# Optimization experiments

Hardware: AMD Instinct MI355X
Metric: run time of the kernel (lower is better)

Reference implementation:

```python
import jax, jax.numpy as jnp
import numpy as np

NUM_EMBEDDINGS = 1024
EMBEDDING_DIM = 64
SCALE = 1.0 / NUM_EMBEDDINGS


def setup_inputs() -> dict:
    key = jax.random.key(0)
    k1, k2 = jax.random.split(key)
    input = jax.random.normal(k1, (16, EMBEDDING_DIM, 64, 64), dtype=jnp.float32)
    # nn.Embedding weight initialized uniform(-scale, scale)
    codebook = jax.random.uniform(k2, (NUM_EMBEDDINGS, EMBEDDING_DIM),
                                  dtype=jnp.float32, minval=-SCALE, maxval=SCALE)
    return {"input": input, "codebook": codebook}


def reference(input, codebook):
    # NCHW -> NHWC, flatten spatial+batch to tokens [N, D]
    x = jnp.transpose(input, (0, 2, 3, 1))           # [B, H, W, D]
    B, H, W, D = x.shape
    flat = x.reshape(-1, D)                          # [N, D]
    dists = (jnp.sum(flat ** 2, axis=1, keepdims=True)
             + jnp.sum(codebook ** 2, axis=1)
             - 2.0 * flat @ codebook.T)              # [N, K]
    idx = jnp.argmin(dists, axis=-1).reshape(B, H, W)  # [B, H, W]
    quantized = codebook[idx]                        # [B, H, W, D]
    return jnp.transpose(quantized, (0, 3, 1, 2))    # [B, D, H, W]
```

## Files before the change

### kernel.cpp

```cpp
#include <hip/hip_runtime.h>

typedef short short8 __attribute__((ext_vector_type(8)));
typedef float f32x4 __attribute__((ext_vector_type(4)));
typedef unsigned long long u64;

#define NE 1024
#define D 64
#define HW 4096
#define NTOK 65536
#define MARGIN 3.0e-3f
#define FLT_MAX_F 3.402823466e+38f

#define WS_BN  0
#define WS_EBF 4096
#define WS_WIN 135168

__device__ __forceinline__ unsigned short f2bf(float f) {
    unsigned u = __float_as_uint(f);
    return (unsigned short)((u + 0x7fffu + ((u >> 16) & 1u)) >> 16);
}

__device__ __forceinline__ unsigned fenc(float f) {
    unsigned u = __float_as_uint(f);
    return (u & 0x80000000u) ? ~u : (u | 0x80000000u);
}
__device__ __forceinline__ float fdec(unsigned u) {
    unsigned v = (u & 0x80000000u) ? (u & 0x7FFFFFFFu) : ~u;
    return __uint_as_float(v);
}

__device__ __forceinline__ float np_sum64_sq(const float* v) {
    float s[8];
#pragma unroll
    for (int j = 0; j < 8; ++j) s[j] = __fmul_rn(v[j], v[j]);
#pragma unroll
    for (int i = 8; i < 64; i += 8) {
#pragma unroll
        for (int j = 0; j < 8; ++j)
            s[j] = __fadd_rn(s[j], __fmul_rn(v[i + j], v[i + j]));
    }
    return __fadd_rn(__fadd_rn(__fadd_rn(s[0], s[1]), __fadd_rn(s[2], s[3])),
                     __fadd_rn(__fadd_rn(s[4], s[5]), __fadd_rn(s[6], s[7])));
}

__global__ __launch_bounds__(256) void kP_prep(
        const float* __restrict__ cb, float* __restrict__ bn,
        unsigned short* __restrict__ ebf, u64* __restrict__ mask,
        unsigned* __restrict__ gmin) {
    const int gid = blockIdx.x * 256 + threadIdx.x;
    int4 z = {0, 0, 0, 0};
    int4* mz = (int4*)mask;
#pragma unroll
    for (int i = 0; i < 8; ++i) mz[(size_t)gid * 8 + i] = z;
    gmin[gid] = 0xFFFFFFFFu;
    ebf[gid] = f2bf(cb[gid]);
    if (gid < NE) {
        float row[D];
        const float4* r4 = reinterpret_cast<const float4*>(cb + (size_t)gid * D);
#pragma unroll
        for (int i = 0; i < 16; ++i) {
            float4 v = r4[i];
            row[4*i+0] = v.x; row[4*i+1] = v.y; row[4*i+2] = v.z; row[4*i+3] = v.w;
        }
        bn[gid] = np_sum64_sq(row);
    }
}

#define K1_HEAD                                                               \
    __shared__ unsigned short ebq[128 * 64];                                  \
    __shared__ float sbn[128];                                                \
    const int sw  = (blockIdx.x & 7) * 512 + (blockIdx.x >> 3);               \
    const int tg  = sw >> 3;                                                  \
    const int c   = sw & 7;                                                   \
    const int tid  = threadIdx.x;                                             \
    const int lane = tid & 63, w = tid >> 6;                                  \
    const int lcol = lane & 15, lhi = lane >> 4, lrow = lhi * 4;              \
    const int tokw = tg * 128 + w * 32;                                       \
    if (tid < 128) sbn[tid] = bn_g[c * 128 + tid];                            \
    const char* src = (const char*)(ebf + (size_t)c * 128 * 64);              \
    _Pragma("unroll")                                                         \
    for (int i = 0; i < 4; ++i) {                                             \
        int L = (tid + i * 256) * 16;                                         \
        int row = L >> 7, wi = L & 127;                                       \
        int4 v = *(const int4*)(src + L);                                     \
        *(int4*)((char*)ebq + row * 128 + (wi ^ ((row & 7) << 4))) = v;       \
    }                                                                         \
    const int b = tokw >> 12, hwb = tokw & 4095;                              \
    const float* xbase = in + (size_t)b * (D * HW);                           \
    const int hw0 = hwb + lcol, hw1 = hw0 + 16;                               \
    const int kb = lhi * 8;                                                   \
    short8 B00, B01, B10, B11;                                                \
    {                                                                         \
        const float* p;                                                       \
        p = xbase + (size_t)kb * HW + hw0;                                    \
        _Pragma("unroll")                                                     \
        for (int j = 0; j < 8; ++j) B00[j] = (short)f2bf(p[(size_t)j * HW]);  \
        p = xbase + (size_t)(kb + 32) * HW + hw0;                             \
        _Pragma("unroll")                                                     \
        for (int j = 0; j < 8; ++j) B01[j] = (short)f2bf(p[(size_t)j * HW]);  \
        p = xbase + (size_t)kb * HW + hw1;                                    \
        _Pragma("unroll")                                                     \
        for (int j = 0; j < 8; ++j) B10[j] = (short)f2bf(p[(size_t)j * HW]);  \
        p = xbase + (size_t)(kb + 32) * HW + hw1;                             \
        _Pragma("unroll")                                                     \
        for (int j = 0; j < 8; ++j) B11[j] = (short)f2bf(p[(size_t)j * HW]);  \
    }                                                                         \
    __syncthreads();                                                          \
    const int swz   = (lcol & 7) << 4;                                        \
    const int aoff0 = lcol * 128 + ((lhi * 16) ^ swz);                        \
    const int aoff1 = lcol * 128 + ((64 + lhi * 16) ^ swz);

#define K1_MFMA(CT)                                                           \
    const char* lp = (const char*)ebq + (CT) * 2048;                          \
    short8 A0 = *(const short8*)(lp + aoff0);                                 \
    short8 A1 = *(const short8*)(lp + aoff1);                                 \
    f32x4 bnv = *(const f32x4*)(sbn + (CT) * 16 + lrow);                      \
    f32x4 acc = {0.f, 0.f, 0.f, 0.f};                                         \
    acc = __builtin_amdgcn_mfma_f32_16x16x32_bf16(A0, B00, acc, 0, 0, 0);     \
    acc = __builtin_amdgcn_mfma_f32_16x16x32_bf16(A1, B01, acc, 0, 0, 0);     \
    f32x4 ac2 = {0.f, 0.f, 0.f, 0.f};                                         \
    ac2 = __builtin_amdgcn_mfma_f32_16x16x32_bf16(A0, B10, ac2, 0, 0, 0);     \
    ac2 = __builtin_amdgcn_mfma_f32_16x16x32_bf16(A1, B11, ac2, 0, 0, 0);

__global__ __launch_bounds__(256, 4) void k1a_min(
        const float* __restrict__ in, const unsigned short* __restrict__ ebf,
        const float* __restrict__ bn_g, unsigned* __restrict__ gmin) {
    K1_HEAD
    float v10 = FLT_MAX_F, v11 = FLT_MAX_F;
#pragma unroll
    for (int ct = 0; ct < 8; ++ct) {
        K1_MFMA(ct)
#pragma unroll
        for (int r = 0; r < 4; ++r) {
            v10 = fminf(v10, __fmaf_rn(-2.0f, acc[r], bnv[r]));
            v11 = fminf(v11, __fmaf_rn(-2.0f, ac2[r], bnv[r]));
        }
    }
    v10 = fminf(v10, __shfl_xor(v10, 16)); v10 = fminf(v10, __shfl_xor(v10, 32));
    v11 = fminf(v11, __shfl_xor(v11, 16)); v11 = fminf(v11, __shfl_xor(v11, 32));
    if (lhi == 0) atomicMin(&gmin[tokw + lcol],      fenc(v10));
    if (lhi == 1) atomicMin(&gmin[tokw + 16 + lcol], fenc(v11));
}

__global__ __launch_bounds__(256, 4) void k1b_mark(
        const float* __restrict__ in, const unsigned short* __restrict__ ebf,
        const float* __restrict__ bn_g, const unsigned* __restrict__ gmin,
        u64* __restrict__ mask) {
    K1_HEAD
    const float thr0 = fdec(gmin[tokw + lcol]) + MARGIN;
    const float thr1 = fdec(gmin[tokw + 16 + lcol]) + MARGIN;
    u64* mrow0 = mask + (size_t)(tokw + lcol) * 16;
    u64* mrow1 = mask + (size_t)(tokw + 16 + lcol) * 16;
#pragma unroll
    for (int ct = 0; ct < 8; ++ct) {
        K1_MFMA(ct)
        const int kg = c * 128 + ct * 16 + lrow;
#pragma unroll
        for (int r = 0; r < 4; ++r) {
            float t0 = __fmaf_rn(-2.0f, acc[r], bnv[r]);
            if (t0 <= thr0) atomicOr(&mrow0[(kg + r) >> 6], 1ull << ((kg + r) & 63));
            float t1 = __fmaf_rn(-2.0f, ac2[r], bnv[r]);
            if (t1 <= thr1) atomicOr(&mrow1[(kg + r) >> 6], 1ull << ((kg + r) & 63));
        }
    }
}

__global__ __launch_bounds__(256, 4) void k2_rerank(
        const float* __restrict__ in, const float* __restrict__ cb,
        const float* __restrict__ bn, const u64* __restrict__ mask,
        unsigned short* __restrict__ win) {
    const int gid = blockIdx.x * 256 + threadIdx.x;
    const int tok = gid >> 3, sub = gid & 7;
    const int b = tok >> 12, hw = tok & 4095;
    const float* x = in + (size_t)b * (D * HW) + hw;
    float xv[D];
#pragma unroll
    for (int d = 0; d < D; ++d) xv[d] = x[(size_t)d * HW];
    const float a = np_sum64_sq(xv);

    u64 best = ~0ull;
    int kp = -1;
    int pos = 0;
    for (int wd = 0; wd < 16; ++wd) {
        u64 m = mask[(size_t)tok * 16 + wd];
        while (m) {
            const int k = wd * 64 + (int)__builtin_ctzll(m);
            m &= m - 1;
            if (((pos++) & 7) != sub) continue;
            if (kp < 0) { kp = k; continue; }
            const float* e0 = cb + (size_t)kp * D;
            const float* e1 = cb + (size_t)k * D;
            float d0 = 0.f, d1 = 0.f;
#pragma unroll
            for (int d = 0; d < 64; ++d) {
                d0 = __fmaf_rn(xv[d], e0[d], d0);
                d1 = __fmaf_rn(xv[d], e1[d], d1);
            }
            float q0 = __fsub_rn(__fadd_rn(a, bn[kp]), __fmul_rn(2.0f, d0));
            float q1 = __fsub_rn(__fadd_rn(a, bn[k]),  __fmul_rn(2.0f, d1));
            u64 key0 = (((u64)__float_as_uint(q0)) << 32) | (unsigned)kp;
            u64 key1 = (((u64)__float_as_uint(q1)) << 32) | (unsigned)k;
            u64 kmin = key0 < key1 ? key0 : key1;
            best = best < kmin ? best : kmin;
            kp = -1;
        }
    }
    if (kp >= 0) {
        const float* e0 = cb + (size_t)kp * D;
        float d0 = 0.f;
#pragma unroll
        for (int d = 0; d < 64; ++d) d0 = __fmaf_rn(xv[d], e0[d], d0);
        float q0 = __fsub_rn(__fadd_rn(a, bn[kp]), __fmul_rn(2.0f, d0));
        u64 key0 = (((u64)__float_as_uint(q0)) << 32) | (unsigned)kp;
        best = best < key0 ? best : key0;
    }
#pragma unroll
    for (int o = 1; o < 8; o <<= 1) {
        u64 v = __shfl_xor(best, o);
        best = best < v ? best : v;
    }
    if (sub == 0) win[tok] = (unsigned short)(best & 0x3FFull);
}

__global__ __launch_bounds__(256) void k3_gather(
        const float* __restrict__ cb, const unsigned short* __restrict__ win,
        float* __restrict__ out) {
    const int gid = blockIdx.x * 256 + threadIdx.x;
    const int tok = gid >> 2, qd = (gid & 3) << 4;
    const int b = tok >> 12, hw = tok & 4095;
    const unsigned k = win[tok];
    const float4* er = reinterpret_cast<const float4*>(cb + (size_t)k * D + qd);
    float* ot = out + (size_t)b * (D * HW) + hw;
#pragma unroll
    for (int i = 0; i < 4; ++i) {
        float4 e = er[i];
        ot[(size_t)(qd + 4*i + 0) * HW] = e.x;
        ot[(size_t)(qd + 4*i + 1) * HW] = e.y;
        ot[(size_t)(qd + 4*i + 2) * HW] = e.z;
        ot[(size_t)(qd + 4*i + 3) * HW] = e.w;
    }
}

extern "C" void kernel_launch(void* const* d_in, const int* in_sizes, int n_in,
                              void* d_out, int out_size, void* d_ws, size_t ws_size,
                              hipStream_t stream) {
    const float* in  = (const float*)d_in[0];
    const float* cb  = (const float*)d_in[1];
    float*       out = (float*)d_out;
    char*        ws  = (char*)d_ws;

    float*          bn   = (float*)(ws + WS_BN);
    unsigned short* ebf  = (unsigned short*)(ws + WS_EBF);
    unsigned short* win  = (unsigned short*)(ws + WS_WIN);
    u64*            mask = (u64*)d_out;
    unsigned*       gmin = (unsigned*)((char*)d_out + 8388608);

    hipLaunchKernelGGL(kP_prep,   dim3(256),  dim3(256), 0, stream, cb, bn, ebf, mask, gmin);
    hipLaunchKernelGGL(k1a_min,   dim3(4096), dim3(256), 0, stream, in, ebf, bn, gmin);
    hipLaunchKernelGGL(k1b_mark,  dim3(4096), dim3(256), 0, stream, in, ebf, bn, gmin, mask);
    hipLaunchKernelGGL(k2_rerank, dim3(2048), dim3(256), 0, stream, in, cb, bn, mask, win);
    hipLaunchKernelGGL(k3_gather, dim3(1024), dim3(256), 0, stream, cb, win, out);
}
```

Measured before the change: 87.03 us.

## Precompute bf16 MFMA input fragments once in prep kernel, reuse in both passes

The prep kernel now converts the NCHW fp32 input into bf16 MFMA B-fragments laid out per thread and stores them in the output buffer. k1a and k1b then read four contiguous short8 values instead of each doing 32 strided fp32 loads plus conversions, and each of the 8 codebook-chunk blocks per token group no longer repeats that conversion. gmin moves to the workspace to make room for the fragments. The cost is one extra write and read of a 8 MB fragment buffer and a larger prep launch.

```diff
diff --git a/kernel.cpp b/kernel.cpp
--- a/kernel.cpp
+++ b/kernel.cpp
@@ -11,9 +11,10 @@
 #define MARGIN 3.0e-3f
 #define FLT_MAX_F 3.402823466e+38f
 
-#define WS_BN  0
-#define WS_EBF 4096
-#define WS_WIN 135168
+#define WS_BN   0
+#define WS_EBF  4096
+#define WS_WIN  135168
+#define WS_GMIN 266240
 
 __device__ __forceinline__ unsigned short f2bf(float f) {
     unsigned u = __float_as_uint(f);
@@ -43,17 +44,15 @@
                      __fadd_rn(__fadd_rn(s[4], s[5]), __fadd_rn(s[6], s[7])));
 }
 
-__global__ __launch_bounds__(256) void kP_prep(
-        const float* __restrict__ cb, float* __restrict__ bn,
-        unsigned short* __restrict__ ebf, u64* __restrict__ mask,
+__global__ __launch_bounds__(256) void kF_prep(
+        const float* __restrict__ in, const float* __restrict__ cb,
+        float* __restrict__ bn, unsigned short* __restrict__ ebf,
+        u64* __restrict__ mask, short8* __restrict__ frag,
         unsigned* __restrict__ gmin) {
     const int gid = blockIdx.x * 256 + threadIdx.x;
-    int4 z = {0, 0, 0, 0};
-    int4* mz = (int4*)mask;
-#pragma unroll
-    for (int i = 0; i < 8; ++i) mz[(size_t)gid * 8 + i] = z;
-    gmin[gid] = 0xFFFFFFFFu;
-    ebf[gid] = f2bf(cb[gid]);
+    ((int4*)mask)[gid] = int4{0, 0, 0, 0};
+    if (gid < NTOK) gmin[gid] = 0xFFFFFFFFu;
+    if (gid < NE * D) ebf[gid] = f2bf(cb[gid]);
     if (gid < NE) {
         float row[D];
         const float4* r4 = reinterpret_cast<const float4*>(cb + (size_t)gid * D);
@@ -64,6 +63,19 @@
         }
         bn[gid] = np_sum64_sq(row);
     }
+    const int slot = gid >> 2, j = gid & 3;
+    const int tid_o = slot & 255, tg = slot >> 8;
+    const int w = tid_o >> 6, lane = tid_o & 63;
+    const int lcol = lane & 15, lhi = lane >> 4;
+    const int tokw = tg * 128 + w * 32;
+    const int b = tokw >> 12, hwb = tokw & 4095;
+    const int hw = hwb + ((j & 2) ? 16 : 0) + lcol;
+    const int kb = lhi * 8 + ((j & 1) ? 32 : 0);
+    const float* p = in + (size_t)b * (D * HW) + (size_t)kb * HW + hw;
+    short8 B;
+#pragma unroll
+    for (int j2 = 0; j2 < 8; ++j2) B[j2] = (short)f2bf(p[(size_t)j2 * HW]);
+    frag[gid] = B;
 }
 
 #define K1_HEAD                                                               \
@@ -85,26 +97,8 @@
         int4 v = *(const int4*)(src + L);                                     \
         *(int4*)((char*)ebq + row * 128 + (wi ^ ((row & 7) << 4))) = v;       \
     }                                                                         \
-    const int b = tokw >> 12, hwb = tokw & 4095;                              \
-    const float* xbase = in + (size_t)b * (D * HW);                           \
-    const int hw0 = hwb + lcol, hw1 = hw0 + 16;                               \
-    const int kb = lhi * 8;                                                   \
-    short8 B00, B01, B10, B11;                                                \
-    {                                                                         \
-        const float* p;                                                       \
-        p = xbase + (size_t)kb * HW + hw0;                                    \
-        _Pragma("unroll")                                                     \
-        for (int j = 0; j < 8; ++j) B00[j] = (short)f2bf(p[(size_t)j * HW]);  \
-        p = xbase + (size_t)(kb + 32) * HW + hw0;                             \
-        _Pragma("unroll")                                                     \
-        for (int j = 0; j < 8; ++j) B01[j] = (short)f2bf(p[(size_t)j * HW]);  \
-        p = xbase + (size_t)kb * HW + hw1;                                    \
-        _Pragma("unroll")                                                     \
-        for (int j = 0; j < 8; ++j) B10[j] = (short)f2bf(p[(size_t)j * HW]);  \
-        p = xbase + (size_t)(kb + 32) * HW + hw1;                             \
-        _Pragma("unroll")                                                     \
-        for (int j = 0; j < 8; ++j) B11[j] = (short)f2bf(p[(size_t)j * HW]);  \
-    }                                                                         \
+    const short8* fp = frag + ((size_t)tg * 256 + tid) * 4;                   \
+    short8 B00 = fp[0], B01 = fp[1], B10 = fp[2], B11 = fp[3];                \
     __syncthreads();                                                          \
     const int swz   = (lcol & 7) << 4;                                        \
     const int aoff0 = lcol * 128 + ((lhi * 16) ^ swz);                        \
@@ -123,8 +117,8 @@
     ac2 = __builtin_amdgcn_mfma_f32_16x16x32_bf16(A1, B11, ac2, 0, 0, 0);
 
 __global__ __launch_bounds__(256, 4) void k1a_min(
-        const float* __restrict__ in, const unsigned short* __restrict__ ebf,
-        const float* __restrict__ bn_g, unsigned* __restrict__ gmin) {
+        const unsigned short* __restrict__ ebf, const float* __restrict__ bn_g,
+        const short8* __restrict__ frag, unsigned* __restrict__ gmin) {
     K1_HEAD
     float v10 = FLT_MAX_F, v11 = FLT_MAX_F;
 #pragma unroll
@@ -143,8 +137,8 @@
 }
 
 __global__ __launch_bounds__(256, 4) void k1b_mark(
-        const float* __restrict__ in, const unsigned short* __restrict__ ebf,
-        const float* __restrict__ bn_g, const unsigned* __restrict__ gmin,
+        const unsigned short* __restrict__ ebf, const float* __restrict__ bn_g,
+        const short8* __restrict__ frag, const unsigned* __restrict__ gmin,
         u64* __restrict__ mask) {
     K1_HEAD
     const float thr0 = fdec(gmin[tokw + lcol]) + MARGIN;
@@ -252,12 +246,13 @@
     float*          bn   = (float*)(ws + WS_BN);
     unsigned short* ebf  = (unsigned short*)(ws + WS_EBF);
     unsigned short* win  = (unsigned short*)(ws + WS_WIN);
+    unsigned*       gmin = (unsigned*)(ws + WS_GMIN);
     u64*            mask = (u64*)d_out;
-    unsigned*       gmin = (unsigned*)((char*)d_out + 8388608);
-
-    hipLaunchKernelGGL(kP_prep,   dim3(256),  dim3(256), 0, stream, cb, bn, ebf, mask, gmin);
-    hipLaunchKernelGGL(k1a_min,   dim3(4096), dim3(256), 0, stream, in, ebf, bn, gmin);
-    hipLaunchKernelGGL(k1b_mark,  dim3(4096), dim3(256), 0, stream, in, ebf, bn, gmin, mask);
+    short8*         frag = (short8*)((char*)d_out + 8388608);
+
+    hipLaunchKernelGGL(kF_prep,   dim3(2048), dim3(256), 0, stream, in, cb, bn, ebf, mask, frag, gmin);
+    hipLaunchKernelGGL(k1a_min,   dim3(4096), dim3(256), 0, stream, ebf, bn, frag, gmin);
+    hipLaunchKernelGGL(k1b_mark,  dim3(4096), dim3(256), 0, stream, ebf, bn, frag, gmin, mask);
     hipLaunchKernelGGL(k2_rerank, dim3(2048), dim3(256), 0, stream, in, cb, bn, mask, win);
     hipLaunchKernelGGL(k3_gather, dim3(1024), dim3(256), 0, stream, cb, win, out);
 }
```

Result: faster. 81.95 us (-5.8%).
